# Performance work log

Measured on AMD Instinct MI355X. Metric: run time of the kernel, lower is better.

## Reference

```python
import jax, jax.numpy as jnp
import numpy as np

T = 256
H, W = 512, 512
SHARPNESS = 100.0
EPS = 1e-6


def setup_inputs() -> dict:
    key = jax.random.key(0)
    k1, k2 = jax.random.split(key)
    verts = jax.random.uniform(k1, (T, 3, 2), dtype=jnp.float32) * 0.5 + 0.25
    colors = jax.random.uniform(k2, (T, 3), dtype=jnp.float32)
    depth = jnp.linspace(-1.0, 1.0, T, dtype=jnp.float32)
    return {"verts": verts, "colors": colors, "depth": depth}


def _edge(px, py, va, vb):
    # va, vb: [T, 2]; px, py: [H, W] -> broadcast to [T, H, W]
    ax = va[:, 0][:, None, None]
    ay = va[:, 1][:, None, None]
    bx = vb[:, 0][:, None, None]
    by = vb[:, 1][:, None, None]
    return (px[None] - ax) * (by - ay) - (py[None] - ay) * (bx - ax)


def reference(verts, colors, depth):
    y = jnp.linspace(0.0, 1.0, H, dtype=verts.dtype)
    x = jnp.linspace(0.0, 1.0, W, dtype=verts.dtype)
    yy, xx = jnp.meshgrid(y, x, indexing="ij")  # [H, W] each

    v0 = verts[:, 0, :]  # [T, 2]
    v1 = verts[:, 1, :]
    v2 = verts[:, 2, :]

    e0 = _edge(xx, yy, v0, v1)  # [T, H, W]
    e1 = _edge(xx, yy, v1, v2)
    e2 = _edge(xx, yy, v2, v0)

    mask = (jax.nn.sigmoid(e0 * SHARPNESS)
            * jax.nn.sigmoid(e1 * SHARPNESS)
            * jax.nn.sigmoid(e2 * SHARPNESS))  # [T, H, W]

    logits = depth[:, None, None] + jnp.log(mask + EPS)  # [T, H, W]
    weights = jax.nn.softmax(logits, axis=0)             # [T, H, W]

    # composite: sum_t colors[t, c] * weights[t, h, w] -> [3, H, W]
    rgb = jnp.einsum("thw,tc->chw", weights, colors)
    return rgb
```

## Files before the change

kernel.cpp:

```cpp
#include <hip/hip_runtime.h>

#define TT 256
#define HH 512
#define WW 512
#define LOG2E 1.44269504088896340736f
#define KS (100.0f * LOG2E)
#define STEP (1.0f / 511.0f)
#define RUN 4
#define CHUNK 32

__global__ __launch_bounds__(256) void tri_setup(
        const float* __restrict__ verts,
        const float* __restrict__ colors,
        const float* __restrict__ depth,
        float* __restrict__ ws) {
    int t = threadIdx.x;

    float v0x = verts[t * 6 + 0], v0y = verts[t * 6 + 1];
    float v1x = verts[t * 6 + 2], v1y = verts[t * 6 + 3];
    float v2x = verts[t * 6 + 4], v2y = verts[t * 6 + 5];

    float dx0 = v1x - v0x, dy0 = v1y - v0y;
    float dx1 = v2x - v1x, dy1 = v2y - v1y;
    float dx2 = v0x - v2x, dy2 = v0y - v2y;
    float c0 = v0y * dx0 - v0x * dy0;
    float c1 = v1y * dx1 - v1x * dy1;
    float c2 = v2y * dx2 - v2x * dy2;

    float expd = __builtin_amdgcn_exp2f(depth[t] * LOG2E);
    float cr = colors[t * 3 + 0], cg = colors[t * 3 + 1], cb = colors[t * 3 + 2];
    float ecr = expd * cr, ecg = expd * cg, ecb = expd * cb;

    float* f = ws + t * 16;
    f[0] = KS * dy0;  f[1] = KS * dx0;  f[2] = KS * c0;
    f[3] = KS * dy1;  f[4] = KS * dx1;  f[5] = KS * c1;
    f[6] = KS * dy2;  f[7] = KS * dx2;  f[8] = KS * c2;
    f[9]  = __builtin_amdgcn_exp2f(STEP * (KS * dx0));
    f[10] = __builtin_amdgcn_exp2f(STEP * (KS * dx1));
    f[11] = __builtin_amdgcn_exp2f(STEP * (KS * dx2));
    f[12] = expd; f[13] = ecr; f[14] = ecg; f[15] = ecb;

    __shared__ float4 red[256];
    red[t] = make_float4(expd * 1e-6f, ecr * 1e-6f, ecg * 1e-6f, ecb * 1e-6f);
    __syncthreads();
    for (int s = 128; s > 0; s >>= 1) {
        if (t < s) {
            float4 a = red[t], b = red[t + s];
            red[t] = make_float4(a.x + b.x, a.y + b.y, a.z + b.z, a.w + b.w);
        }
        __syncthreads();
    }
    if (t == 0) {
        ws[16 * TT + 0] = red[0].x;
        ws[16 * TT + 1] = red[0].y;
        ws[16 * TT + 2] = red[0].z;
        ws[16 * TT + 3] = red[0].w;
    }
}

__global__ __launch_bounds__(512, 8) void tri_render(
        const float* __restrict__ ws,
        float* __restrict__ out) {
    __shared__ float4 s_part[4][RUN][64];

    int tid  = threadIdx.x;
    int lane = tid & 63;
    int wave = __builtin_amdgcn_readfirstlane(tid >> 6);

    int bx = blockIdx.x & 7;
    int by = blockIdx.x >> 3;

    float px  = (float)(bx * 64 + lane) * STEP;
    float py0 = (float)(by * RUN) * STEP;

    float acc[RUN][4];
    #pragma unroll
    for (int i = 0; i < RUN; ++i) {
        acc[i][0] = 0.0f; acc[i][1] = 0.0f; acc[i][2] = 0.0f; acc[i][3] = 0.0f;
    }

    const float* tbase = ws + wave * (CHUNK * 16);

    #pragma unroll 2
    for (int j = 0; j < CHUNK; ++j) {
        const float* tp = tbase + (j << 4);
        float Dy0 = tp[0],  Dx0 = tp[1],  C0 = tp[2];
        float Dy1 = tp[3],  Dx1 = tp[4],  C1 = tp[5];
        float Dy2 = tp[6],  Dx2 = tp[7],  C2 = tp[8];

        float n0 = fmaf(py0, Dx0, -C0);  n0 = fmaf(-px, Dy0, n0);
        float n1 = fmaf(py0, Dx1, -C1);  n1 = fmaf(-px, Dy1, n1);
        float n2 = fmaf(py0, Dx2, -C2);  n2 = fmaf(-px, Dy2, n2);

        float nmax = fmaxf(fmaxf(n0, n1), n2);
        if (__all(nmax > 34.0f)) continue;

        float u0 = __builtin_amdgcn_exp2f(n0);
        float u1 = __builtin_amdgcn_exp2f(n1);
        float u2 = __builtin_amdgcn_exp2f(n2);
        float k0 = tp[9], k1 = tp[10], k2 = tp[11];
        float ce = tp[12], cr = tp[13], cg = tp[14], cb = tp[15];

        #pragma unroll
        for (int i = 0; i < RUN / 2; ++i) {
            float a  = u1 + 1.0f;
            float PA = fmaf(u0, a, a);
            PA = fmaf(u2, PA, PA);
            PA = fminf(PA, 1e18f);
            u0 *= k0; u1 *= k1; u2 *= k2;
            a = u1 + 1.0f;
            float PB = fmaf(u0, a, a);
            PB = fmaf(u2, PB, PB);
            PB = fminf(PB, 1e18f);
            if (i != RUN / 2 - 1) { u0 *= k0; u1 *= k1; u2 *= k2; }

            float rinv = __builtin_amdgcn_rcpf(PA * PB);
            float wA = rinv * PB;
            float wB = rinv * PA;

            acc[2*i][0]   = fmaf(wA, ce, acc[2*i][0]);
            acc[2*i+1][0] = fmaf(wB, ce, acc[2*i+1][0]);
            acc[2*i][1]   = fmaf(wA, cr, acc[2*i][1]);
            acc[2*i+1][1] = fmaf(wB, cr, acc[2*i+1][1]);
            acc[2*i][2]   = fmaf(wA, cg, acc[2*i][2]);
            acc[2*i+1][2] = fmaf(wB, cg, acc[2*i+1][2]);
            acc[2*i][3]   = fmaf(wA, cb, acc[2*i][3]);
            acc[2*i+1][3] = fmaf(wB, cb, acc[2*i+1][3]);
        }
    }

    if (wave >= 4) {
        #pragma unroll
        for (int i = 0; i < RUN; ++i)
            s_part[wave - 4][i][lane] =
                make_float4(acc[i][0], acc[i][1], acc[i][2], acc[i][3]);
    }
    __syncthreads();
    if (wave < 4) {
        #pragma unroll
        for (int i = 0; i < RUN; ++i) {
            float4 v = s_part[wave][i][lane];
            v.x += acc[i][0]; v.y += acc[i][1];
            v.z += acc[i][2]; v.w += acc[i][3];
            s_part[wave][i][lane] = v;
        }
    }
    __syncthreads();

    if (tid < 64 * RUN) {
        const float* base = ws + 16 * TT;
        float b0 = base[0], b1 = base[1], b2 = base[2], b3 = base[3];

        int i = tid >> 6, l = tid & 63;
        float4 v0 = s_part[0][i][l];
        float4 v1 = s_part[1][i][l];
        float4 v2 = s_part[2][i][l];
        float4 v3 = s_part[3][i][l];
        float sum = b0 + ((v0.x + v1.x) + (v2.x + v3.x));
        float r   = b1 + ((v0.y + v1.y) + (v2.y + v3.y));
        float g   = b2 + ((v0.z + v1.z) + (v2.z + v3.z));
        float bch = b3 + ((v0.w + v1.w) + (v2.w + v3.w));
        float inv = 1.0f / sum;
        int gy = by * RUN + i;
        int gx = bx * 64 + l;
        int pix = gy * WW + gx;
        out[pix]               = r   * inv;
        out[HH * WW + pix]     = g   * inv;
        out[2 * HH * WW + pix] = bch * inv;
    }
}

extern "C" void kernel_launch(void* const* d_in, const int* in_sizes, int n_in,
                              void* d_out, int out_size, void* d_ws, size_t ws_size,
                              hipStream_t stream) {
    const float* verts  = (const float*)d_in[0];
    const float* colors = (const float*)d_in[1];
    const float* depth  = (const float*)d_in[2];
    float* out = (float*)d_out;
    float* ws  = (float*)d_ws;

    tri_setup<<<dim3(1), dim3(256), 0, stream>>>(verts, colors, depth, ws);
    tri_render<<<dim3((WW / 64) * (HH / RUN)), dim3(512), 0, stream>>>(ws, out);
}
```

Measured before the change: 36.41 us.

## Fuse triangle setup into render kernel with per-block LDS records

Removes the separate single-block setup kernel and has every render block recompute the per-triangle records into shared memory, with the epsilon sum done by an LDS load plus a wave shuffle reduction. The per-triangle loop now reads float4 records from LDS instead of scalar global loads. It also drops the wave-uniform early-exit test that skipped triangles whose edge terms are all large. This saves one kernel launch and its dependency gap, at the cost of redundant setup work in every block, about 20 KB of extra LDS per block that may limit occupancy, and evaluating every triangle.

Measured after the change: 31.44 us. 1.16x faster.

```diff
diff --git a/kernel.cpp b/kernel.cpp
--- a/kernel.cpp
+++ b/kernel.cpp
@@ -9,63 +9,62 @@
 #define RUN 4
 #define CHUNK 32
 
-__global__ __launch_bounds__(256) void tri_setup(
+__global__ __launch_bounds__(512, 8) void tri_render(
         const float* __restrict__ verts,
         const float* __restrict__ colors,
         const float* __restrict__ depth,
-        float* __restrict__ ws) {
-    int t = threadIdx.x;
-
-    float v0x = verts[t * 6 + 0], v0y = verts[t * 6 + 1];
-    float v1x = verts[t * 6 + 2], v1y = verts[t * 6 + 3];
-    float v2x = verts[t * 6 + 4], v2y = verts[t * 6 + 5];
-
-    float dx0 = v1x - v0x, dy0 = v1y - v0y;
-    float dx1 = v2x - v1x, dy1 = v2y - v1y;
-    float dx2 = v0x - v2x, dy2 = v0y - v2y;
-    float c0 = v0y * dx0 - v0x * dy0;
-    float c1 = v1y * dx1 - v1x * dy1;
-    float c2 = v2y * dx2 - v2x * dy2;
-
-    float expd = __builtin_amdgcn_exp2f(depth[t] * LOG2E);
-    float cr = colors[t * 3 + 0], cg = colors[t * 3 + 1], cb = colors[t * 3 + 2];
-    float ecr = expd * cr, ecg = expd * cg, ecb = expd * cb;
-
-    float* f = ws + t * 16;
-    f[0] = KS * dy0;  f[1] = KS * dx0;  f[2] = KS * c0;
-    f[3] = KS * dy1;  f[4] = KS * dx1;  f[5] = KS * c1;
-    f[6] = KS * dy2;  f[7] = KS * dx2;  f[8] = KS * c2;
-    f[9]  = __builtin_amdgcn_exp2f(STEP * (KS * dx0));
-    f[10] = __builtin_amdgcn_exp2f(STEP * (KS * dx1));
-    f[11] = __builtin_amdgcn_exp2f(STEP * (KS * dx2));
-    f[12] = expd; f[13] = ecr; f[14] = ecg; f[15] = ecb;
-
-    __shared__ float4 red[256];
-    red[t] = make_float4(expd * 1e-6f, ecr * 1e-6f, ecg * 1e-6f, ecb * 1e-6f);
-    __syncthreads();
-    for (int s = 128; s > 0; s >>= 1) {
-        if (t < s) {
-            float4 a = red[t], b = red[t + s];
-            red[t] = make_float4(a.x + b.x, a.y + b.y, a.z + b.z, a.w + b.w);
-        }
-        __syncthreads();
-    }
-    if (t == 0) {
-        ws[16 * TT + 0] = red[0].x;
-        ws[16 * TT + 1] = red[0].y;
-        ws[16 * TT + 2] = red[0].z;
-        ws[16 * TT + 3] = red[0].w;
-    }
-}
-
-__global__ __launch_bounds__(512, 8) void tri_render(
-        const float* __restrict__ ws,
         float* __restrict__ out) {
+    __shared__ float4 s_rec[TT][4];
+    __shared__ float4 s_eps[TT];
     __shared__ float4 s_part[4][RUN][64];
 
     int tid  = threadIdx.x;
     int lane = tid & 63;
     int wave = __builtin_amdgcn_readfirstlane(tid >> 6);
+
+    if (tid < TT) {
+        int t = tid;
+        float v0x = verts[t * 6 + 0], v0y = verts[t * 6 + 1];
+        float v1x = verts[t * 6 + 2], v1y = verts[t * 6 + 3];
+        float v2x = verts[t * 6 + 4], v2y = verts[t * 6 + 5];
+
+        float dx0 = v1x - v0x, dy0 = v1y - v0y;
+        float dx1 = v2x - v1x, dy1 = v2y - v1y;
+        float dx2 = v0x - v2x, dy2 = v0y - v2y;
+        float c0 = v0y * dx0 - v0x * dy0;
+        float c1 = v1y * dx1 - v1x * dy1;
+        float c2 = v2y * dx2 - v2x * dy2;
+
+        float expd = __builtin_amdgcn_exp2f(depth[t] * LOG2E);
+        float cr = colors[t * 3 + 0], cg = colors[t * 3 + 1], cb = colors[t * 3 + 2];
+
+        s_rec[t][0] = make_float4(KS * dy0, KS * dx0, KS * c0, KS * dy1);
+        s_rec[t][1] = make_float4(KS * dx1, KS * c1, KS * dy2, KS * dx2);
+        s_rec[t][2] = make_float4(KS * c2,
+                                  __builtin_amdgcn_exp2f(STEP * (KS * dx0)),
+                                  __builtin_amdgcn_exp2f(STEP * (KS * dx1)),
+                                  __builtin_amdgcn_exp2f(STEP * (KS * dx2)));
+        s_rec[t][3] = make_float4(expd, expd * cr, expd * cg, expd * cb);
+        float se = expd * 1e-6f;
+        s_eps[t] = make_float4(se, se * cr, se * cg, se * cb);
+    }
+    __syncthreads();
+
+    float4 e0 = s_eps[lane];
+    float4 e1 = s_eps[lane + 64];
+    float4 e2 = s_eps[lane + 128];
+    float4 e3 = s_eps[lane + 192];
+    float b0 = (e0.x + e1.x) + (e2.x + e3.x);
+    float b1 = (e0.y + e1.y) + (e2.y + e3.y);
+    float b2 = (e0.z + e1.z) + (e2.z + e3.z);
+    float b3 = (e0.w + e1.w) + (e2.w + e3.w);
+    #pragma unroll
+    for (int d = 1; d < 64; d <<= 1) {
+        b0 += __shfl_xor(b0, d, 64);
+        b1 += __shfl_xor(b1, d, 64);
+        b2 += __shfl_xor(b2, d, 64);
+        b3 += __shfl_xor(b3, d, 64);
+    }
 
     int bx = blockIdx.x & 7;
     int by = blockIdx.x >> 3;
@@ -79,27 +78,23 @@
         acc[i][0] = 0.0f; acc[i][1] = 0.0f; acc[i][2] = 0.0f; acc[i][3] = 0.0f;
     }
 
-    const float* tbase = ws + wave * (CHUNK * 16);
+    const float4* rec = &s_rec[wave * CHUNK][0];
 
-    #pragma unroll 2
+    #pragma unroll 1
     for (int j = 0; j < CHUNK; ++j) {
-        const float* tp = tbase + (j << 4);
-        float Dy0 = tp[0],  Dx0 = tp[1],  C0 = tp[2];
-        float Dy1 = tp[3],  Dx1 = tp[4],  C1 = tp[5];
-        float Dy2 = tp[6],  Dx2 = tp[7],  C2 = tp[8];
+        float4 q0 = rec[j * 4 + 0];
+        float4 q1 = rec[j * 4 + 1];
+        float4 q2 = rec[j * 4 + 2];
+        float4 q3 = rec[j * 4 + 3];
 
-        float n0 = fmaf(py0, Dx0, -C0);  n0 = fmaf(-px, Dy0, n0);
-        float n1 = fmaf(py0, Dx1, -C1);  n1 = fmaf(-px, Dy1, n1);
-        float n2 = fmaf(py0, Dx2, -C2);  n2 = fmaf(-px, Dy2, n2);
-
-        float nmax = fmaxf(fmaxf(n0, n1), n2);
-        if (__all(nmax > 34.0f)) continue;
-
+        float n0 = fmaf(py0, q0.y, -q0.z);  n0 = fmaf(-px, q0.x, n0);
+        float n1 = fmaf(py0, q1.x, -q1.y);  n1 = fmaf(-px, q0.w, n1);
+        float n2 = fmaf(py0, q1.w, -q2.x);  n2 = fmaf(-px, q1.z, n2);
         float u0 = __builtin_amdgcn_exp2f(n0);
         float u1 = __builtin_amdgcn_exp2f(n1);
         float u2 = __builtin_amdgcn_exp2f(n2);
-        float k0 = tp[9], k1 = tp[10], k2 = tp[11];
-        float ce = tp[12], cr = tp[13], cg = tp[14], cb = tp[15];
+        float k0 = q2.y, k1 = q2.z, k2 = q2.w;
+        float ce = q3.x, cr = q3.y, cg = q3.z, cb = q3.w;
 
         #pragma unroll
         for (int i = 0; i < RUN / 2; ++i) {
@@ -128,6 +123,7 @@
             acc[2*i+1][3] = fmaf(wB, cb, acc[2*i+1][3]);
         }
     }
+    __syncthreads();
 
     if (wave >= 4) {
         #pragma unroll
@@ -148,9 +144,6 @@
     __syncthreads();
 
     if (tid < 64 * RUN) {
-        const float* base = ws + 16 * TT;
-        float b0 = base[0], b1 = base[1], b2 = base[2], b3 = base[3];
-
         int i = tid >> 6, l = tid & 63;
         float4 v0 = s_part[0][i][l];
         float4 v1 = s_part[1][i][l];
@@ -177,8 +170,7 @@
     const float* colors = (const float*)d_in[1];
     const float* depth  = (const float*)d_in[2];
     float* out = (float*)d_out;
-    float* ws  = (float*)d_ws;
 
-    tri_setup<<<dim3(1), dim3(256), 0, stream>>>(verts, colors, depth, ws);
-    tri_render<<<dim3((WW / 64) * (HH / RUN)), dim3(512), 0, stream>>>(ws, out);
+    tri_render<<<dim3((WW / 64) * (HH / RUN)), dim3(512), 0, stream>>>(
+        verts, colors, depth, out);
 }
```

## Replace wave-level skip with clamped exponents and per-pixel reciprocal

Applied to the files above, without the earlier changes.

Removes the wave-uniform early-out test for triangles far from the pixel strip. Each exponent is now clamped to 30 so the product cannot overflow, which also drops the 1e18 clamp. The shared reciprocal over pixel pairs is replaced by one reciprocal per pixel, and the triangle loop is no longer unrolled. This trades the divergent branch and extra multiplies for always doing full work on every triangle, and changes precision for pixels well outside a triangle.

New measurement: 34.77 us. 4.5% less time.

```diff
diff --git a/kernel.cpp b/kernel.cpp
--- a/kernel.cpp
+++ b/kernel.cpp
@@ -29,7 +29,6 @@
 
     float expd = __builtin_amdgcn_exp2f(depth[t] * LOG2E);
     float cr = colors[t * 3 + 0], cg = colors[t * 3 + 1], cb = colors[t * 3 + 2];
-    float ecr = expd * cr, ecg = expd * cg, ecb = expd * cb;
 
     float* f = ws + t * 16;
     f[0] = KS * dy0;  f[1] = KS * dx0;  f[2] = KS * c0;
@@ -38,10 +37,11 @@
     f[9]  = __builtin_amdgcn_exp2f(STEP * (KS * dx0));
     f[10] = __builtin_amdgcn_exp2f(STEP * (KS * dx1));
     f[11] = __builtin_amdgcn_exp2f(STEP * (KS * dx2));
-    f[12] = expd; f[13] = ecr; f[14] = ecg; f[15] = ecb;
+    f[12] = expd; f[13] = expd * cr; f[14] = expd * cg; f[15] = expd * cb;
 
     __shared__ float4 red[256];
-    red[t] = make_float4(expd * 1e-6f, ecr * 1e-6f, ecg * 1e-6f, ecb * 1e-6f);
+    red[t] = make_float4(expd * 1e-6f, expd * cr * 1e-6f,
+                         expd * cg * 1e-6f, expd * cb * 1e-6f);
     __syncthreads();
     for (int s = 128; s > 0; s >>= 1) {
         if (t < s) {
@@ -81,51 +81,33 @@
 
     const float* tbase = ws + wave * (CHUNK * 16);
 
-    #pragma unroll 2
+    #pragma unroll 1
     for (int j = 0; j < CHUNK; ++j) {
         const float* tp = tbase + (j << 4);
         float Dy0 = tp[0],  Dx0 = tp[1],  C0 = tp[2];
         float Dy1 = tp[3],  Dx1 = tp[4],  C1 = tp[5];
         float Dy2 = tp[6],  Dx2 = tp[7],  C2 = tp[8];
+        float k0  = tp[9],  k1  = tp[10], k2 = tp[11];
+        float ce  = tp[12], cr  = tp[13], cg = tp[14], cb = tp[15];
 
-        float n0 = fmaf(py0, Dx0, -C0);  n0 = fmaf(-px, Dy0, n0);
-        float n1 = fmaf(py0, Dx1, -C1);  n1 = fmaf(-px, Dy1, n1);
-        float n2 = fmaf(py0, Dx2, -C2);  n2 = fmaf(-px, Dy2, n2);
-
-        float nmax = fmaxf(fmaxf(n0, n1), n2);
-        if (__all(nmax > 34.0f)) continue;
-
+        float n0 = fmaf(py0, Dx0, -C0);  n0 = fmaf(-px, Dy0, n0);  n0 = fminf(n0, 30.0f);
+        float n1 = fmaf(py0, Dx1, -C1);  n1 = fmaf(-px, Dy1, n1);  n1 = fminf(n1, 30.0f);
+        float n2 = fmaf(py0, Dx2, -C2);  n2 = fmaf(-px, Dy2, n2);  n2 = fminf(n2, 30.0f);
         float u0 = __builtin_amdgcn_exp2f(n0);
         float u1 = __builtin_amdgcn_exp2f(n1);
         float u2 = __builtin_amdgcn_exp2f(n2);
-        float k0 = tp[9], k1 = tp[10], k2 = tp[11];
-        float ce = tp[12], cr = tp[13], cg = tp[14], cb = tp[15];
 
         #pragma unroll
-        for (int i = 0; i < RUN / 2; ++i) {
-            float a  = u1 + 1.0f;
-            float PA = fmaf(u0, a, a);
-            PA = fmaf(u2, PA, PA);
-            PA = fminf(PA, 1e18f);
-            u0 *= k0; u1 *= k1; u2 *= k2;
-            a = u1 + 1.0f;
-            float PB = fmaf(u0, a, a);
-            PB = fmaf(u2, PB, PB);
-            PB = fminf(PB, 1e18f);
-            if (i != RUN / 2 - 1) { u0 *= k0; u1 *= k1; u2 *= k2; }
-
-            float rinv = __builtin_amdgcn_rcpf(PA * PB);
-            float wA = rinv * PB;
-            float wB = rinv * PA;
-
-            acc[2*i][0]   = fmaf(wA, ce, acc[2*i][0]);
-            acc[2*i+1][0] = fmaf(wB, ce, acc[2*i+1][0]);
-            acc[2*i][1]   = fmaf(wA, cr, acc[2*i][1]);
-            acc[2*i+1][1] = fmaf(wB, cr, acc[2*i+1][1]);
-            acc[2*i][2]   = fmaf(wA, cg, acc[2*i][2]);
-            acc[2*i+1][2] = fmaf(wB, cg, acc[2*i+1][2]);
-            acc[2*i][3]   = fmaf(wA, cb, acc[2*i][3]);
-            acc[2*i+1][3] = fmaf(wB, cb, acc[2*i+1][3]);
+        for (int i = 0; i < RUN; ++i) {
+            float a = u1 + 1.0f;
+            float P = fmaf(u0, a, a);
+            P = fmaf(u2, P, P);
+            float w = __builtin_amdgcn_rcpf(P);
+            if (i != RUN - 1) { u0 *= k0; u1 *= k1; u2 *= k2; }
+            acc[i][0] = fmaf(w, ce, acc[i][0]);
+            acc[i][1] = fmaf(w, cr, acc[i][1]);
+            acc[i][2] = fmaf(w, cg, acc[i][2]);
+            acc[i][3] = fmaf(w, cb, acc[i][3]);
         }
     }
 
```
